# Kernel tuning notes

Hardware: AMD Instinct MI355X
Metric: run time of the kernel (lower is better)

The kernel has to match this reference:

```python
import jax, jax.numpy as jnp
import numpy as np

B, D = 1024, 512


def setup_inputs() -> dict:
    key = jax.random.key(0)
    k1, k2, k3 = jax.random.split(key, 3)
    x = jax.random.normal(k1, (B, D), dtype=jnp.float32)
    x_dot = jax.random.normal(k2, (B, D), dtype=jnp.float32)
    # linear score network weight: s(x) = x @ W^T  (scaled for sane magnitudes)
    W = jax.random.normal(k3, (D, D), dtype=jnp.float32) / np.sqrt(D).astype(np.float32)
    return {"x": x, "x_dot": x_dot, "W": W}


def reference(x, x_dot, W):
    # s(x): [b, d]
    s = x @ W.T
    d = x.shape[1]
    # g(x) = I + s s^T : [b, d, d]  (faithful to the original bmm formulation)
    G = jnp.eye(d, dtype=x.dtype)[None, :, :] + s[:, :, None] * s[:, None, :]
    # kinetic energy: x_dot^T G x_dot : [b]
    return jnp.einsum('bi,bij,bj->b', x_dot, G, x_dot)
```

## Files before the change

### kernel.cpp

```cpp
#include <hip/hip_runtime.h>

#define BB 1024
#define DD 512
#define BTILE 32
#define JTILE 128
#define ICH 64
#define NIC (DD / ICH)
#define NP ((DD / JTILE) * NIC)

__global__ __launch_bounds__(256, 4) void stm_main_kernel(
    const float* __restrict__ x, const float* __restrict__ xdot,
    const float* __restrict__ W, float* __restrict__ ws_t) {
  __shared__ float xd_t[ICH][BTILE];
  __shared__ float w_s[ICH][JTILE];

  const int tid = threadIdx.x;
  const int b0 = blockIdx.x * BTILE;
  const int j0 = blockIdx.y * JTILE;
  const int i0 = blockIdx.z * ICH;
  const int tb = tid >> 5;
  const int tj = tid & 31;

  {
    const int row = tid & 31;
    const int f4 = tid >> 5;
    const float4* src = (const float4*)(xdot + (size_t)(b0 + row) * DD + i0);
#pragma unroll
    for (int p = 0; p < 2; ++p) {
      const int c4 = f4 + p * 8;
      float4 v = src[c4];
      const int c = c4 * 4;
      xd_t[c + 0][row] = v.x; xd_t[c + 1][row] = v.y;
      xd_t[c + 2][row] = v.z; xd_t[c + 3][row] = v.w;
    }
  }
  {
#pragma unroll
    for (int v = 0; v < 8; ++v) {
      const int f4 = tid + v * 256;
      const int ii = f4 >> 5, jj4 = f4 & 31;
      *((float4*)&w_s[ii][jj4 * 4]) =
          ((const float4*)(W + (size_t)(i0 + ii) * DD + j0))[jj4];
    }
  }
  __syncthreads();

  float acc[4][4] = {};
#pragma unroll
  for (int i = 0; i < ICH; ++i) {
    const float4 xd = *(const float4*)&xd_t[i][tb * 4];
    const float4 w  = *(const float4*)&w_s[i][tj * 4];
    acc[0][0] += xd.x * w.x; acc[0][1] += xd.x * w.y;
    acc[0][2] += xd.x * w.z; acc[0][3] += xd.x * w.w;
    acc[1][0] += xd.y * w.x; acc[1][1] += xd.y * w.y;
    acc[1][2] += xd.y * w.z; acc[1][3] += xd.y * w.w;
    acc[2][0] += xd.z * w.x; acc[2][1] += xd.z * w.y;
    acc[2][2] += xd.z * w.z; acc[2][3] += xd.z * w.w;
    acc[3][0] += xd.w * w.x; acc[3][1] += xd.w * w.y;
    acc[3][2] += xd.w * w.z; acc[3][3] += xd.w * w.w;
  }

  float tp[4];
#pragma unroll
  for (int r = 0; r < 4; ++r) {
    const float4 xv =
        ((const float4*)(x + (size_t)(b0 + tb * 4 + r) * DD + j0))[tj];
    tp[r] = acc[r][0] * xv.x + acc[r][1] * xv.y +
            acc[r][2] * xv.z + acc[r][3] * xv.w;
  }
#pragma unroll
  for (int off = 16; off >= 1; off >>= 1) {
#pragma unroll
    for (int r = 0; r < 4; ++r) tp[r] += __shfl_xor(tp[r], off);
  }
  if (tj == 0) {
    const int p = blockIdx.y * NIC + blockIdx.z;
    *(float4*)(ws_t + (size_t)p * BB + b0 + tb * 4) =
        make_float4(tp[0], tp[1], tp[2], tp[3]);
  }
}

__global__ __launch_bounds__(256) void stm_final_kernel(
    const float* __restrict__ xdot, const float* __restrict__ ws_t,
    float* __restrict__ out) {
  const int tid = threadIdx.x;
  const int wv = tid >> 6, ln = tid & 63;
  const int b = blockIdx.x * 4 + wv;
  const float4* xd4 = (const float4*)(xdot + (size_t)b * DD);
  const float4 a = xd4[ln];
  const float4 c = xd4[64 + ln];
  float n = a.x * a.x + a.y * a.y + a.z * a.z + a.w * a.w +
            c.x * c.x + c.y * c.y + c.z * c.z + c.w * c.w;
  float t = (ln < NP) ? ws_t[(size_t)ln * BB + b] : 0.f;
#pragma unroll
  for (int off = 32; off >= 1; off >>= 1) {
    n += __shfl_xor(n, off);
    t += __shfl_xor(t, off);
  }
  if (ln == 0) out[b] = n + t * t;
}

extern "C" void kernel_launch(void* const* d_in, const int* in_sizes, int n_in,
                              void* d_out, int out_size, void* d_ws, size_t ws_size,
                              hipStream_t stream) {
  const float* x    = (const float*)d_in[0];
  const float* xdot = (const float*)d_in[1];
  const float* W    = (const float*)d_in[2];
  float* ws = (float*)d_ws;
  float* out = (float*)d_out;

  dim3 g1(BB / BTILE, DD / JTILE, NIC);
  stm_main_kernel<<<g1, 256, 0, stream>>>(x, xdot, W, ws);
  stm_final_kernel<<<BB / 4, 256, 0, stream>>>(xdot, ws, out);
}
```

Measured before the change: 68.83 us.

## Fuse xdot norm into main kernel and simplify final reduction

The squared norm of x_dot is now computed from the values the main kernel already loads into shared memory, and the partial sums are written to the workspace. This removes the second full read of x_dot from the final kernel. The final kernel becomes a per-thread column sum over partials launched with only 4 blocks. The x loads are also hoisted ahead of the barrier so they overlap with the inner product, at the cost of extra registers.

```diff
diff --git a/kernel.cpp b/kernel.cpp
--- a/kernel.cpp
+++ b/kernel.cpp
@@ -6,7 +6,8 @@
 #define JTILE 128
 #define ICH 64
 #define NIC (DD / ICH)
-#define NP ((DD / JTILE) * NIC)
+#define NTP ((DD / JTILE) * NIC)
+#define NNP (NIC * 4)
 
 __global__ __launch_bounds__(256, 4) void stm_main_kernel(
     const float* __restrict__ x, const float* __restrict__ xdot,
@@ -21,6 +22,7 @@
   const int tb = tid >> 5;
   const int tj = tid & 31;
 
+  float nrm = 0.f;
   {
     const int row = tid & 31;
     const int f4 = tid >> 5;
@@ -29,6 +31,7 @@
     for (int p = 0; p < 2; ++p) {
       const int c4 = f4 + p * 8;
       float4 v = src[c4];
+      nrm += v.x * v.x + v.y * v.y + v.z * v.z + v.w * v.w;
       const int c = c4 * 4;
       xd_t[c + 0][row] = v.x; xd_t[c + 1][row] = v.y;
       xd_t[c + 2][row] = v.z; xd_t[c + 3][row] = v.w;
@@ -43,6 +46,19 @@
           ((const float4*)(W + (size_t)(i0 + ii) * DD + j0))[jj4];
     }
   }
+
+  if (blockIdx.y == 0) {
+    nrm += __shfl_xor(nrm, 32);
+    const int wv = tid >> 6, ln = tid & 63;
+    if (ln < 32)
+      ws_t[(size_t)(NTP + blockIdx.z * 4 + wv) * BB + b0 + ln] = nrm;
+  }
+
+  float4 xv[4];
+#pragma unroll
+  for (int r = 0; r < 4; ++r)
+    xv[r] = ((const float4*)(x + (size_t)(b0 + tb * 4 + r) * DD + j0))[tj];
+
   __syncthreads();
 
   float acc[4][4] = {};
@@ -62,12 +78,9 @@
 
   float tp[4];
 #pragma unroll
-  for (int r = 0; r < 4; ++r) {
-    const float4 xv =
-        ((const float4*)(x + (size_t)(b0 + tb * 4 + r) * DD + j0))[tj];
-    tp[r] = acc[r][0] * xv.x + acc[r][1] * xv.y +
-            acc[r][2] * xv.z + acc[r][3] * xv.w;
-  }
+  for (int r = 0; r < 4; ++r)
+    tp[r] = acc[r][0] * xv[r].x + acc[r][1] * xv[r].y +
+            acc[r][2] * xv[r].z + acc[r][3] * xv[r].w;
 #pragma unroll
   for (int off = 16; off >= 1; off >>= 1) {
 #pragma unroll
@@ -81,23 +94,14 @@
 }
 
 __global__ __launch_bounds__(256) void stm_final_kernel(
-    const float* __restrict__ xdot, const float* __restrict__ ws_t,
-    float* __restrict__ out) {
-  const int tid = threadIdx.x;
-  const int wv = tid >> 6, ln = tid & 63;
-  const int b = blockIdx.x * 4 + wv;
-  const float4* xd4 = (const float4*)(xdot + (size_t)b * DD);
-  const float4 a = xd4[ln];
-  const float4 c = xd4[64 + ln];
-  float n = a.x * a.x + a.y * a.y + a.z * a.z + a.w * a.w +
-            c.x * c.x + c.y * c.y + c.z * c.z + c.w * c.w;
-  float t = (ln < NP) ? ws_t[(size_t)ln * BB + b] : 0.f;
+    const float* __restrict__ ws_t, float* __restrict__ out) {
+  const int b = blockIdx.x * 256 + threadIdx.x;
+  float t = 0.f, n = 0.f;
 #pragma unroll
-  for (int off = 32; off >= 1; off >>= 1) {
-    n += __shfl_xor(n, off);
-    t += __shfl_xor(t, off);
-  }
-  if (ln == 0) out[b] = n + t * t;
+  for (int p = 0; p < NTP; ++p) t += ws_t[(size_t)p * BB + b];
+#pragma unroll
+  for (int p = 0; p < NNP; ++p) n += ws_t[(size_t)(NTP + p) * BB + b];
+  out[b] = n + t * t;
 }
 
 extern "C" void kernel_launch(void* const* d_in, const int* in_sizes, int n_in,
@@ -111,5 +115,5 @@
 
   dim3 g1(BB / BTILE, DD / JTILE, NIC);
   stm_main_kernel<<<g1, 256, 0, stream>>>(x, xdot, W, ws);
-  stm_final_kernel<<<BB / 4, 256, 0, stream>>>(xdot, ws, out);
+  stm_final_kernel<<<BB / 256, 256, 0, stream>>>(ws, out);
 }
```

Result: no change. 69.01 us, median of 2 (+0.3%).
